# Optimization experiments

Measured on AMD Instinct MI355X. Metric: run time of the kernel, lower is better.

## Reference

```python
import jax, jax.numpy as jnp
import numpy as np

B, S, D, H, DH = 2, 2048, 2048, 16, 128
ROT_DIM = 128
ROT_BASE = 10000.0
ATTN_SCALE = float(np.sqrt(DH))


def _sin_cos_rotary(n_ctx, rotary_dim, base):
    pos = jnp.arange(n_ctx, dtype=jnp.float32)
    dim = jnp.arange(rotary_dim // 2, dtype=jnp.float32)
    freq = base ** (dim / (rotary_dim / 2))
    freq = jnp.concatenate([freq, freq])  # non-adjacent pairs: '(2 d)' layout
    angles = pos[:, None] / freq[None, :]  # [n_ctx, rotary_dim]
    return jnp.sin(angles), jnp.cos(angles)


def _rotate_every_two(x):
    # non-adjacent-pairs rotation: [-x2, x1] on halves of last dim
    d = x.shape[-1]
    return jnp.concatenate([-x[..., d // 2:], x[..., :d // 2]], axis=-1)


def _apply_rotary(x, sin, cos):
    # x: [batch, pos, head, d_head]
    n = x.shape[1]
    x_rot = x[..., :ROT_DIM]
    x_pass = x[..., ROT_DIM:]
    c = cos[:n][None, :, None, :]
    s = sin[:n][None, :, None, :]
    x_rotated = x_rot * c + _rotate_every_two(x_rot) * s
    return jnp.concatenate([x_rotated, x_pass], axis=-1)


def setup_inputs() -> dict:
    key = jax.random.key(0)
    ks = jax.random.split(key, 8)
    init = 0.02
    return {
        'query_input': jax.random.normal(ks[0], (B, S, D), jnp.float32),
        'key_input': jax.random.normal(ks[1], (B, S, D), jnp.float32),
        'value_input': jax.random.normal(ks[2], (B, S, D), jnp.float32),
        'W_Q': jax.random.normal(ks[3], (H, D, DH), jnp.float32) * init,
        'W_K': jax.random.normal(ks[4], (H, D, DH), jnp.float32) * init,
        'W_V': jax.random.normal(ks[5], (H, D, DH), jnp.float32) * init,
        'W_O': jax.random.normal(ks[6], (H, DH, D), jnp.float32) * init,
        'b_Q': jnp.zeros((H, DH), jnp.float32),
        'b_K': jnp.zeros((H, DH), jnp.float32),
        'b_V': jnp.zeros((H, DH), jnp.float32),
        'b_O': jnp.zeros((D,), jnp.float32),
    }


def reference(query_input, key_input, value_input, W_Q, W_K, W_V, W_O, b_Q, b_K, b_V, b_O):
    # QKV projections: [b, pos, d_model] x [h, d_model, d_head] -> [b, pos, h, d_head]
    q = jnp.einsum('bpd,hde->bphe', query_input, W_Q) + b_Q
    k = jnp.einsum('bpd,hde->bphe', key_input, W_K) + b_K
    v = jnp.einsum('bpd,hde->bphe', value_input, W_V) + b_V

    sin, cos = _sin_cos_rotary(S, ROT_DIM, ROT_BASE)
    q = _apply_rotary(q, sin, cos)
    k = _apply_rotary(k, sin, cos)

    # attention scores [b, h, q_pos, k_pos]
    scores = jnp.einsum('bqhe,bkhe->bhqk', q, k) / ATTN_SCALE
    causal = jnp.tril(jnp.ones((S, S), bool))
    scores = jnp.where(causal[None, None], scores, -jnp.inf)
    pattern = jax.nn.softmax(scores, axis=-1)
    pattern = jnp.where(jnp.isnan(pattern), jnp.zeros_like(pattern), pattern)

    z = jnp.einsum('bhqk,bkhe->bqhe', pattern, v)
    out = jnp.einsum('bqhe,hed->bqd', z, W_O) + b_O
    return out
```

## Files before the change

kernel.cpp:

```cpp
#include <hip/hip_runtime.h>
#include <hip/hip_bf16.h>
#include <cmath>

typedef __bf16 bf16;
typedef __bf16 bf16x8 __attribute__((ext_vector_type(8)));
typedef __bf16 bf16x4 __attribute__((ext_vector_type(4)));
typedef float  f32x4  __attribute__((ext_vector_type(4)));


__global__ void prep_kernel(const float* __restrict__ qin, const float* __restrict__ kin,
                            const float* __restrict__ vin,
                            const float* __restrict__ WQ, const float* __restrict__ WK,
                            const float* __restrict__ WV, const float* __restrict__ WO,
                            bf16* __restrict__ XQ, bf16* __restrict__ XK, bf16* __restrict__ XV,
                            bf16* __restrict__ WQT, bf16* __restrict__ WKT,
                            bf16* __restrict__ WVT, bf16* __restrict__ WOT) {
    int y = blockIdx.y;
    int o = blockIdx.x * 256 + threadIdx.x;
    if (y == 0) {
        int i = o * 2;
        float2 a = *(const float2*)(qin + i);
        float2 b = *(const float2*)(kin + i);
        float2 c = *(const float2*)(vin + i);
        bf16 ra[2] = { (bf16)a.x, (bf16)a.y };
        bf16 rb[2] = { (bf16)b.x, (bf16)b.y };
        bf16 rc[2] = { (bf16)c.x, (bf16)c.y };
        *(short*)&XQ[i] = *(short*)&ra[0]; *(short*)&XQ[i+1] = *(short*)&ra[1];
        *(short*)&XK[i] = *(short*)&rb[0]; *(short*)&XK[i+1] = *(short*)&rb[1];
        *(short*)&XV[i] = *(short*)&rc[0]; *(short*)&XV[i+1] = *(short*)&rc[1];
    } else if (y < 4) {
        const float* W = (y == 1) ? WQ : (y == 2) ? WK : WV;
        bf16* Wt       = (y == 1) ? WQT : (y == 2) ? WKT : WVT;
        int d = o & 2047;
        int he = o >> 11;
        int e = he & 127, h = he >> 7;
        Wt[o] = (bf16)W[(h << 18) + (d << 7) + e];
    } else {
        int he = o & 2047;
        int d = o >> 11;
        WOT[o] = (bf16)WO[(he << 11) + d];
    }
}

__launch_bounds__(256)
__global__ void qkv_gemm_kernel(const bf16* __restrict__ XQ, const bf16* __restrict__ XK,
                                const bf16* __restrict__ XV,
                                const bf16* __restrict__ WQT, const bf16* __restrict__ WKT,
                                const bf16* __restrict__ WVT,
                                const float* __restrict__ bQ, const float* __restrict__ bK,
                                const float* __restrict__ bV,
                                bf16* __restrict__ QB, bf16* __restrict__ KB,
                                bf16* __restrict__ VT) {
    __shared__ __align__(16) bf16 As[128 * 32];
    __shared__ __align__(16) bf16 Bs[128 * 32];
    __shared__ __align__(16) bf16 Cs[64 * 136];
    const int z = blockIdx.z;
    const bf16* A  = (z == 0) ? XQ  : (z == 1) ? XK  : XV;
    const bf16* Bm = (z == 0) ? WQT : (z == 1) ? WKT : WVT;
    const float* bias = (z == 0) ? bQ : (z == 1) ? bK : bV;

    const int tid = threadIdx.x;
    const int w = tid >> 6, lane = tid & 63;
    const int quad = lane >> 4, l16 = lane & 15;
    const int wm = w & 1, wn = w >> 1;
    const int m_base = blockIdx.x << 7, n_base = blockIdx.y << 7;

    const int srow = lane >> 2;
    const int scol = (lane & 3) << 3;
    const int ab0 = w * 2, ab1 = w * 2 + 1;
    const bf16* gA0 = A  + (long)(m_base + ab0 * 16 + srow) * 2048 + scol;
    const bf16* gA1 = A  + (long)(m_base + ab1 * 16 + srow) * 2048 + scol;
    const bf16* gB0 = Bm + (long)(n_base + ab0 * 16 + srow) * 2048 + scol;
    const bf16* gB1 = Bm + (long)(n_base + ab1 * 16 + srow) * 2048 + scol;
    bf16* lA0 = &As[ab0 * 512];
    bf16* lA1 = &As[ab1 * 512];
    bf16* lB0 = &Bs[ab0 * 512];
    bf16* lB1 = &Bs[ab1 * 512];

    f32x4 acc[4][4] = {};

    for (int k0 = 0; k0 < 2048; k0 += 32) {
        __builtin_amdgcn_global_load_lds((const __attribute__((address_space(1))) void*)(gA0 + k0),
                                         (__attribute__((address_space(3))) void*)lA0, 16, 0, 0);
        __builtin_amdgcn_global_load_lds((const __attribute__((address_space(1))) void*)(gA1 + k0),
                                         (__attribute__((address_space(3))) void*)lA1, 16, 0, 0);
        __builtin_amdgcn_global_load_lds((const __attribute__((address_space(1))) void*)(gB0 + k0),
                                         (__attribute__((address_space(3))) void*)lB0, 16, 0, 0);
        __builtin_amdgcn_global_load_lds((const __attribute__((address_space(1))) void*)(gB1 + k0),
                                         (__attribute__((address_space(3))) void*)lB1, 16, 0, 0);
        __syncthreads();

        bf16x8 af[4], bfr[4];
#pragma unroll
        for (int mt = 0; mt < 4; mt++)
            af[mt] = *(const bf16x8*)&As[((wm * 64 + mt * 16 + l16) << 5) + (quad << 3)];
#pragma unroll
        for (int nt = 0; nt < 4; nt++) {
            int nrow = wn * 32 + (nt & 1) * 16 + (nt >> 1) * 64 + l16;
            bfr[nt] = *(const bf16x8*)&Bs[(nrow << 5) + (quad << 3)];
        }
#pragma unroll
        for (int mt = 0; mt < 4; mt++)
#pragma unroll
            for (int nt = 0; nt < 4; nt++)
                acc[mt][nt] = __builtin_amdgcn_mfma_f32_16x16x32_bf16(af[mt], bfr[nt], acc[mt][nt], 0, 0, 0);
        __syncthreads();
    }

    const int bq = m_base >> 11;
    const int h  = n_base >> 7;
    const long obase = ((long)(bq * 16 + h)) << 18;

    if (z <= 1) {
        bf16* O = (z == 0) ? QB : KB;
        const float scl = (z == 0) ? 0.08838834764831845f : 1.0f;
#pragma unroll
        for (int nt = 0; nt < 2; nt++) {
            const int e_lo = wn * 32 + nt * 16 + l16;
            const float bv_lo = bias[n_base + e_lo];
            const float bv_hi = bias[n_base + e_lo + 64];
            const float inv_freq = exp2f((float)e_lo * -0.20762050593046f);
#pragma unroll
            for (int mt = 0; mt < 4; mt++) {
#pragma unroll
                for (int r = 0; r < 4; r++) {
                    int s = (m_base & 2047) + wm * 64 + mt * 16 + quad * 4 + r;
                    float sn, cs;
                    __sincosf((float)s * inv_freq, &sn, &cs);
                    float x0 = acc[mt][nt][r]     + bv_lo;
                    float x1 = acc[mt][nt + 2][r] + bv_hi;
                    O[obase + ((long)s << 7) + e_lo]      = (bf16)((x0 * cs - x1 * sn) * scl);
                    O[obase + ((long)s << 7) + e_lo + 64] = (bf16)((x1 * cs + x0 * sn) * scl);
                }
            }
        }
    } else {
#pragma unroll
        for (int eh = 0; eh < 2; eh++) {
#pragma unroll
            for (int nt2 = 0; nt2 < 2; nt2++) {
                const int nt = eh * 2 + nt2;
                const int e_l = wn * 32 + nt2 * 16 + l16;
                const float bv = bias[n_base + eh * 64 + e_l];
#pragma unroll
                for (int mt = 0; mt < 4; mt++) {
                    int s0 = wm * 64 + mt * 16 + quad * 4;
                    bf16x4 pk = { (bf16)(acc[mt][nt][0] + bv), (bf16)(acc[mt][nt][1] + bv),
                                  (bf16)(acc[mt][nt][2] + bv), (bf16)(acc[mt][nt][3] + bv) };
                    *(bf16x4*)&Cs[e_l * 136 + s0] = pk;
                }
            }
            __syncthreads();
            {
                const int e_l = tid >> 2;
                const int sq  = (tid & 3) << 5;
                const int e   = eh * 64 + e_l;
                const long vb = obase + ((long)e << 11) + (m_base & 2047) + sq;
#pragma unroll
                for (int j = 0; j < 4; j++)
                    *(bf16x8*)&VT[vb + j * 8] = *(const bf16x8*)&Cs[e_l * 136 + sq + j * 8];
            }
            __syncthreads();
        }
    }
}

__launch_bounds__(256, 3)
__global__ void flash_kernel(const bf16* __restrict__ Q, const bf16* __restrict__ K,
                             const bf16* __restrict__ Vt, bf16* __restrict__ Z) {
    __shared__ __align__(16) bf16 Ks[64 * 136];
    __shared__ __align__(16) bf16 Vs[128 * 72];
    __shared__ __align__(16) bf16 Ps[64 * 72];
    const int tid = threadIdx.x, w = tid >> 6, lane = tid & 63;
    const int quad = lane >> 4, l16 = lane & 15;
    const int n = blockIdx.x;
    const int bh = (n & 7) | (((n >> 3) & 3) << 3);
    const int qt = 31 - (n >> 5);
    const int b = bh >> 4, h = bh & 15;
    const long qk_base = (long)bh << 18;
    const int qbase = qt << 6;
    const float FM = 12.0f;

    const int kr_row = tid >> 4;
    const int kr_col = (tid & 15) << 3;
    const int vr_row = tid >> 3;
    const int vr_col = (tid & 7) << 3;
    const bf16* Kg = K  + qk_base + (long)kr_row * 128 + kr_col;
    const bf16* Vg = Vt + qk_base + (long)vr_row * 2048 + vr_col;

    bf16x8 qf[4];
#pragma unroll
    for (int ks = 0; ks < 4; ks++)
        qf[ks] = *(const bf16x8*)(Q + qk_base + ((long)(qbase + w * 16 + l16) << 7) + ks * 32 + (quad << 3));

    bf16x8 va[4], ka[4], vb2[4], kb[4];
#pragma unroll
    for (int p = 0; p < 4; p++) va[p] = *(const bf16x8*)(Vg + (long)p * 65536);
#pragma unroll
    for (int p = 0; p < 4; p++) ka[p] = *(const bf16x8*)(Kg + (long)(p * 16) * 128);

    f32x4 o[8] = {};
    float lsum[4] = {0.f, 0.f, 0.f, 0.f};

    for (int kt = 0; kt <= qt; kt++) {
#pragma unroll
        for (int p = 0; p < 4; p++)
            *(bf16x8*)&Vs[(p * 32 + vr_row) * 72 + vr_col] = va[p];
#pragma unroll
        for (int p = 0; p < 4; p++)
            *(bf16x8*)&Ks[(p * 16 + kr_row) * 136 + kr_col] = ka[p];
        if (kt < qt) {
            const long koff = (long)(kt + 1) * 64;
#pragma unroll
            for (int p = 0; p < 4; p++) vb2[p] = *(const bf16x8*)(Vg + (long)p * 65536 + koff);
#pragma unroll
            for (int p = 0; p < 4; p++) kb[p] = *(const bf16x8*)(Kg + (koff + p * 16) * 128);
        }
        __syncthreads();

        f32x4 sc[4] = {};
#pragma unroll
        for (int nt = 0; nt < 4; nt++)
#pragma unroll
            for (int ks = 0; ks < 4; ks++) {
                bf16x8 kf = *(const bf16x8*)&Ks[(nt * 16 + l16) * 136 + ks * 32 + (quad << 3)];
                sc[nt] = __builtin_amdgcn_mfma_f32_16x16x32_bf16(qf[ks], kf, sc[nt], 0, 0, 0);
            }

        if (kt == qt) {
#pragma unroll
            for (int nt = 0; nt < 4; nt++)
#pragma unroll
                for (int r = 0; r < 4; r++) {
                    int qrow = qbase + w * 16 + quad * 4 + r;
                    int kv = (qt << 6) + nt * 16 + l16;
                    if (kv > qrow) sc[nt][r] = -3.0e38f;
                }
        }

#pragma unroll
        for (int nt = 0; nt < 4; nt++)
#pragma unroll
            for (int r = 0; r < 4; r++) {
                float p = __expf(sc[nt][r] - FM);
                lsum[r] += p;
                Ps[(w * 16 + quad * 4 + r) * 72 + nt * 16 + l16] = (bf16)p;
            }

#pragma unroll
        for (int kk = 0; kk < 2; kk++) {
            bf16x8 pf = *(const bf16x8*)&Ps[(w * 16 + l16) * 72 + kk * 32 + (quad << 3)];
#pragma unroll
            for (int dt = 0; dt < 8; dt++) {
                bf16x8 vf = *(const bf16x8*)&Vs[(dt * 16 + l16) * 72 + kk * 32 + (quad << 3)];
                o[dt] = __builtin_amdgcn_mfma_f32_16x16x32_bf16(pf, vf, o[dt], 0, 0, 0);
            }
        }
        __syncthreads();

#pragma unroll
        for (int p = 0; p < 4; p++) va[p] = vb2[p];
#pragma unroll
        for (int p = 0; p < 4; p++) ka[p] = kb[p];
    }

#pragma unroll
    for (int r = 0; r < 4; r++) {
        float l = lsum[r];
        l += __shfl_xor(l, 1);
        l += __shfl_xor(l, 2);
        l += __shfl_xor(l, 4);
        l += __shfl_xor(l, 8);
        float inv = 1.f / l;
        int qrow = qbase + w * 16 + quad * 4 + r;
        long zr = ((long)(b * 2048 + qrow) << 11) + h * 128;
#pragma unroll
        for (int dt = 0; dt < 8; dt++)
            Z[zr + dt * 16 + l16] = (bf16)(o[dt][r] * inv);
    }
}

__launch_bounds__(256)
__global__ void gemm_o_kernel(const bf16* __restrict__ A, const bf16* __restrict__ Bm,
                              const float* __restrict__ bias, float* __restrict__ Of) {
    __shared__ __align__(16) bf16 As[128 * 32];
    __shared__ __align__(16) bf16 Bs[128 * 32];
    const int tid = threadIdx.x;
    const int w = tid >> 6, lane = tid & 63;
    const int quad = lane >> 4, l16 = lane & 15;
    const int wm = w & 1, wn = w >> 1;
    const int m_base = blockIdx.x << 7, n_base = blockIdx.y << 7;

    const int srow = lane >> 2;
    const int scol = (lane & 3) << 3;
    const int ab0 = w * 2, ab1 = w * 2 + 1;
    const bf16* gA0 = A  + (long)(m_base + ab0 * 16 + srow) * 2048 + scol;
    const bf16* gA1 = A  + (long)(m_base + ab1 * 16 + srow) * 2048 + scol;
    const bf16* gB0 = Bm + (long)(n_base + ab0 * 16 + srow) * 2048 + scol;
    const bf16* gB1 = Bm + (long)(n_base + ab1 * 16 + srow) * 2048 + scol;
    bf16* lA0 = &As[ab0 * 512];
    bf16* lA1 = &As[ab1 * 512];
    bf16* lB0 = &Bs[ab0 * 512];
    bf16* lB1 = &Bs[ab1 * 512];

    f32x4 acc[4][4] = {};

    for (int k0 = 0; k0 < 2048; k0 += 32) {
        __builtin_amdgcn_global_load_lds((const __attribute__((address_space(1))) void*)(gA0 + k0),
                                         (__attribute__((address_space(3))) void*)lA0, 16, 0, 0);
        __builtin_amdgcn_global_load_lds((const __attribute__((address_space(1))) void*)(gA1 + k0),
                                         (__attribute__((address_space(3))) void*)lA1, 16, 0, 0);
        __builtin_amdgcn_global_load_lds((const __attribute__((address_space(1))) void*)(gB0 + k0),
                                         (__attribute__((address_space(3))) void*)lB0, 16, 0, 0);
        __builtin_amdgcn_global_load_lds((const __attribute__((address_space(1))) void*)(gB1 + k0),
                                         (__attribute__((address_space(3))) void*)lB1, 16, 0, 0);
        __syncthreads();

        bf16x8 af[4], bfr[4];
#pragma unroll
        for (int mt = 0; mt < 4; mt++)
            af[mt] = *(const bf16x8*)&As[((wm * 64 + mt * 16 + l16) << 5) + (quad << 3)];
#pragma unroll
        for (int nt = 0; nt < 4; nt++)
            bfr[nt] = *(const bf16x8*)&Bs[((wn * 64 + nt * 16 + l16) << 5) + (quad << 3)];
#pragma unroll
        for (int mt = 0; mt < 4; mt++)
#pragma unroll
            for (int nt = 0; nt < 4; nt++)
                acc[mt][nt] = __builtin_amdgcn_mfma_f32_16x16x32_bf16(af[mt], bfr[nt], acc[mt][nt], 0, 0, 0);
        __syncthreads();
    }

#pragma unroll
    for (int nt = 0; nt < 4; nt++) {
        int col = n_base + wn * 64 + nt * 16 + l16;
        float bv = bias[col];
#pragma unroll
        for (int mt = 0; mt < 4; mt++) {
#pragma unroll
            for (int r = 0; r < 4; r++) {
                int row = m_base + wm * 64 + mt * 16 + quad * 4 + r;
                Of[((long)row << 11) + col] = acc[mt][nt][r] + bv;
            }
        }
    }
}

extern "C" void kernel_launch(void* const* d_in, const int* in_sizes, int n_in,
                              void* d_out, int out_size, void* d_ws, size_t ws_size,
                              hipStream_t stream) {
    (void)in_sizes; (void)n_in; (void)out_size; (void)ws_size;
    const float* qin = (const float*)d_in[0];
    const float* kin = (const float*)d_in[1];
    const float* vin = (const float*)d_in[2];
    const float* WQ  = (const float*)d_in[3];
    const float* WK  = (const float*)d_in[4];
    const float* WV  = (const float*)d_in[5];
    const float* WO  = (const float*)d_in[6];
    const float* bQ  = (const float*)d_in[7];
    const float* bK  = (const float*)d_in[8];
    const float* bV  = (const float*)d_in[9];
    const float* bO  = (const float*)d_in[10];
    float* out = (float*)d_out;

    bf16* ws = (bf16*)d_ws;
    bf16* XQ  = ws + 0L;
    bf16* XK  = ws + 8388608L;
    bf16* XV  = ws + 16777216L;
    bf16* WQT = ws + 25165824L;
    bf16* WKT = ws + 29360128L;
    bf16* WVT = ws + 33554432L;
    bf16* WOT = ws + 37748736L;
    bf16* QB  = ws + 41943040L;
    bf16* KB  = ws + 50331648L;
    bf16* VT  = ws + 58720256L;
    bf16* Z   = XQ;

    prep_kernel<<<dim3(16384, 5), 256, 0, stream>>>(qin, kin, vin, WQ, WK, WV, WO,
                                                    XQ, XK, XV, WQT, WKT, WVT, WOT);
    qkv_gemm_kernel<<<dim3(32, 16, 3), 256, 0, stream>>>(XQ, XK, XV, WQT, WKT, WVT,
                                                         bQ, bK, bV, QB, KB, VT);
    flash_kernel<<<1024, 256, 0, stream>>>(QB, KB, VT, Z);
    gemm_o_kernel<<<dim3(32, 16), 256, 0, stream>>>(Z, WOT, bO, out);
}
```

Before: 476.2 us.

## Split prep into vectorized convert and tiled transpose; register-prefetch padded GEMM tiles

The single prep kernel is replaced by two kernels. One converts the activations to bf16 with float4 loads. The other transposes the weights through a padded shared-memory tile so that both reads and writes are coalesced, replacing the strided per-element gathers. The QKV and output GEMMs drop the direct global-to-LDS loads and instead prefetch the next K-slice into registers while computing the current one. They store into LDS rows padded to 40 elements to avoid bank conflicts and declare launch bounds asking for 3 blocks per CU. This costs more registers and an extra store into LDS.

```diff
diff --git a/kernel.cpp b/kernel.cpp
--- a/kernel.cpp
+++ b/kernel.cpp
@@ -8,41 +8,70 @@
 typedef float  f32x4  __attribute__((ext_vector_type(4)));
 
 
-__global__ void prep_kernel(const float* __restrict__ qin, const float* __restrict__ kin,
-                            const float* __restrict__ vin,
-                            const float* __restrict__ WQ, const float* __restrict__ WK,
-                            const float* __restrict__ WV, const float* __restrict__ WO,
-                            bf16* __restrict__ XQ, bf16* __restrict__ XK, bf16* __restrict__ XV,
-                            bf16* __restrict__ WQT, bf16* __restrict__ WKT,
-                            bf16* __restrict__ WVT, bf16* __restrict__ WOT) {
-    int y = blockIdx.y;
-    int o = blockIdx.x * 256 + threadIdx.x;
-    if (y == 0) {
-        int i = o * 2;
-        float2 a = *(const float2*)(qin + i);
-        float2 b = *(const float2*)(kin + i);
-        float2 c = *(const float2*)(vin + i);
-        bf16 ra[2] = { (bf16)a.x, (bf16)a.y };
-        bf16 rb[2] = { (bf16)b.x, (bf16)b.y };
-        bf16 rc[2] = { (bf16)c.x, (bf16)c.y };
-        *(short*)&XQ[i] = *(short*)&ra[0]; *(short*)&XQ[i+1] = *(short*)&ra[1];
-        *(short*)&XK[i] = *(short*)&rb[0]; *(short*)&XK[i+1] = *(short*)&rb[1];
-        *(short*)&XV[i] = *(short*)&rc[0]; *(short*)&XV[i+1] = *(short*)&rc[1];
-    } else if (y < 4) {
-        const float* W = (y == 1) ? WQ : (y == 2) ? WK : WV;
-        bf16* Wt       = (y == 1) ? WQT : (y == 2) ? WKT : WVT;
-        int d = o & 2047;
-        int he = o >> 11;
-        int e = he & 127, h = he >> 7;
-        Wt[o] = (bf16)W[(h << 18) + (d << 7) + e];
+__global__ void xcvt_kernel(const float* __restrict__ a, const float* __restrict__ b,
+                            const float* __restrict__ c,
+                            bf16* __restrict__ oa, bf16* __restrict__ ob, bf16* __restrict__ oc) {
+    int i = (blockIdx.x * 256 + threadIdx.x) * 4;
+    float4 va = *(const float4*)(a + i);
+    float4 vb = *(const float4*)(b + i);
+    float4 vc = *(const float4*)(c + i);
+    bf16x4 ra = { (bf16)va.x, (bf16)va.y, (bf16)va.z, (bf16)va.w };
+    bf16x4 rb = { (bf16)vb.x, (bf16)vb.y, (bf16)vb.z, (bf16)vb.w };
+    bf16x4 rc = { (bf16)vc.x, (bf16)vc.y, (bf16)vc.z, (bf16)vc.w };
+    *(bf16x4*)(oa + i) = ra;
+    *(bf16x4*)(ob + i) = rb;
+    *(bf16x4*)(oc + i) = rc;
+}
+
+__global__ void wtr_kernel(const float* __restrict__ WQ, const float* __restrict__ WK,
+                           const float* __restrict__ WV, const float* __restrict__ WO,
+                           bf16* __restrict__ WQT, bf16* __restrict__ WKT,
+                           bf16* __restrict__ WVT, bf16* __restrict__ WOT) {
+    __shared__ float T[64 * 65];
+    const int z = blockIdx.y;
+    const int bx = blockIdx.x;
+    const int tid = threadIdx.x;
+    const int tr = tid >> 4;
+    const int tc = (tid & 15) * 4;
+
+    const float* src; bf16* dst;
+    long sbase, dbase; int sRS;
+    if (z < 3) {
+        src = (z == 0) ? WQ : (z == 1) ? WK : WV;
+        dst = (z == 0) ? WQT : (z == 1) ? WKT : WVT;
+        int h = bx >> 6, rem = bx & 63;
+        int d0 = (rem >> 1) << 6, e0 = (rem & 1) << 6;
+        sbase = (long)h * 262144 + (long)d0 * 128 + e0;
+        sRS = 128;
+        dbase = (long)(h * 128 + e0) * 2048 + d0;
     } else {
-        int he = o & 2047;
-        int d = o >> 11;
-        WOT[o] = (bf16)WO[(he << 11) + d];
-    }
-}
-
-__launch_bounds__(256)
+        src = WO; dst = WOT;
+        int a0 = (bx >> 5) << 6, b0 = (bx & 31) << 6;
+        sbase = (long)a0 * 2048 + b0;
+        sRS = 2048;
+        dbase = (long)b0 * 2048 + a0;
+    }
+
+#pragma unroll
+    for (int p = 0; p < 4; p++) {
+        int r = p * 16 + tr;
+        float4 v = *(const float4*)(src + sbase + (long)r * sRS + tc);
+        T[r * 65 + tc]     = v.x;
+        T[r * 65 + tc + 1] = v.y;
+        T[r * 65 + tc + 2] = v.z;
+        T[r * 65 + tc + 3] = v.w;
+    }
+    __syncthreads();
+#pragma unroll
+    for (int p = 0; p < 4; p++) {
+        int rr = p * 16 + tr;
+        bf16x4 o = { (bf16)T[tc * 65 + rr],       (bf16)T[(tc + 1) * 65 + rr],
+                     (bf16)T[(tc + 2) * 65 + rr], (bf16)T[(tc + 3) * 65 + rr] };
+        *(bf16x4*)(dst + dbase + (long)rr * 2048 + tc) = o;
+    }
+}
+
+__launch_bounds__(256, 3)
 __global__ void qkv_gemm_kernel(const bf16* __restrict__ XQ, const bf16* __restrict__ XK,
                                 const bf16* __restrict__ XV,
                                 const bf16* __restrict__ WQT, const bf16* __restrict__ WKT,
@@ -51,8 +80,8 @@
                                 const float* __restrict__ bV,
                                 bf16* __restrict__ QB, bf16* __restrict__ KB,
                                 bf16* __restrict__ VT) {
-    __shared__ __align__(16) bf16 As[128 * 32];
-    __shared__ __align__(16) bf16 Bs[128 * 32];
+    __shared__ __align__(16) bf16 As[128 * 40];
+    __shared__ __align__(16) bf16 Bs[128 * 40];
     __shared__ __align__(16) bf16 Cs[64 * 136];
     const int z = blockIdx.z;
     const bf16* A  = (z == 0) ? XQ  : (z == 1) ? XK  : XV;
@@ -65,39 +94,42 @@
     const int wm = w & 1, wn = w >> 1;
     const int m_base = blockIdx.x << 7, n_base = blockIdx.y << 7;
 
-    const int srow = lane >> 2;
-    const int scol = (lane & 3) << 3;
-    const int ab0 = w * 2, ab1 = w * 2 + 1;
-    const bf16* gA0 = A  + (long)(m_base + ab0 * 16 + srow) * 2048 + scol;
-    const bf16* gA1 = A  + (long)(m_base + ab1 * 16 + srow) * 2048 + scol;
-    const bf16* gB0 = Bm + (long)(n_base + ab0 * 16 + srow) * 2048 + scol;
-    const bf16* gB1 = Bm + (long)(n_base + ab1 * 16 + srow) * 2048 + scol;
-    bf16* lA0 = &As[ab0 * 512];
-    bf16* lA1 = &As[ab1 * 512];
-    bf16* lB0 = &Bs[ab0 * 512];
-    bf16* lB1 = &Bs[ab1 * 512];
+    const int srow = tid >> 2;
+    const int scol = (tid & 3) << 3;
+    const bf16* gA = A  + (long)(m_base + srow) * 2048 + scol;
+    const bf16* gB = Bm + (long)(n_base + srow) * 2048 + scol;
 
     f32x4 acc[4][4] = {};
+    bf16x8 ar[2], br[2], arn[2], brn[2];
+#pragma unroll
+    for (int p = 0; p < 2; p++) {
+        ar[p] = *(const bf16x8*)(gA + (long)p * 64 * 2048);
+        br[p] = *(const bf16x8*)(gB + (long)p * 64 * 2048);
+    }
 
     for (int k0 = 0; k0 < 2048; k0 += 32) {
-        __builtin_amdgcn_global_load_lds((const __attribute__((address_space(1))) void*)(gA0 + k0),
-                                         (__attribute__((address_space(3))) void*)lA0, 16, 0, 0);
-        __builtin_amdgcn_global_load_lds((const __attribute__((address_space(1))) void*)(gA1 + k0),
-                                         (__attribute__((address_space(3))) void*)lA1, 16, 0, 0);
-        __builtin_amdgcn_global_load_lds((const __attribute__((address_space(1))) void*)(gB0 + k0),
-                                         (__attribute__((address_space(3))) void*)lB0, 16, 0, 0);
-        __builtin_amdgcn_global_load_lds((const __attribute__((address_space(1))) void*)(gB1 + k0),
-                                         (__attribute__((address_space(3))) void*)lB1, 16, 0, 0);
+#pragma unroll
+        for (int p = 0; p < 2; p++) {
+            *(bf16x8*)&As[(p * 64 + srow) * 40 + scol] = ar[p];
+            *(bf16x8*)&Bs[(p * 64 + srow) * 40 + scol] = br[p];
+        }
+        if (k0 + 32 < 2048) {
+#pragma unroll
+            for (int p = 0; p < 2; p++) {
+                arn[p] = *(const bf16x8*)(gA + (long)p * 64 * 2048 + k0 + 32);
+                brn[p] = *(const bf16x8*)(gB + (long)p * 64 * 2048 + k0 + 32);
+            }
+        }
         __syncthreads();
 
         bf16x8 af[4], bfr[4];
 #pragma unroll
         for (int mt = 0; mt < 4; mt++)
-            af[mt] = *(const bf16x8*)&As[((wm * 64 + mt * 16 + l16) << 5) + (quad << 3)];
+            af[mt] = *(const bf16x8*)&As[(wm * 64 + mt * 16 + l16) * 40 + (quad << 3)];
 #pragma unroll
         for (int nt = 0; nt < 4; nt++) {
             int nrow = wn * 32 + (nt & 1) * 16 + (nt >> 1) * 64 + l16;
-            bfr[nt] = *(const bf16x8*)&Bs[(nrow << 5) + (quad << 3)];
+            bfr[nt] = *(const bf16x8*)&Bs[nrow * 40 + (quad << 3)];
         }
 #pragma unroll
         for (int mt = 0; mt < 4; mt++)
@@ -105,6 +137,9 @@
             for (int nt = 0; nt < 4; nt++)
                 acc[mt][nt] = __builtin_amdgcn_mfma_f32_16x16x32_bf16(af[mt], bfr[nt], acc[mt][nt], 0, 0, 0);
         __syncthreads();
+
+#pragma unroll
+        for (int p = 0; p < 2; p++) { ar[p] = arn[p]; br[p] = brn[p]; }
     }
 
     const int bq = m_base >> 11;
@@ -280,55 +315,61 @@
     }
 }
 
-__launch_bounds__(256)
+__launch_bounds__(256, 3)
 __global__ void gemm_o_kernel(const bf16* __restrict__ A, const bf16* __restrict__ Bm,
                               const float* __restrict__ bias, float* __restrict__ Of) {
-    __shared__ __align__(16) bf16 As[128 * 32];
-    __shared__ __align__(16) bf16 Bs[128 * 32];
+    __shared__ __align__(16) bf16 As[128 * 40];
+    __shared__ __align__(16) bf16 Bs[128 * 40];
     const int tid = threadIdx.x;
     const int w = tid >> 6, lane = tid & 63;
     const int quad = lane >> 4, l16 = lane & 15;
     const int wm = w & 1, wn = w >> 1;
     const int m_base = blockIdx.x << 7, n_base = blockIdx.y << 7;
 
-    const int srow = lane >> 2;
-    const int scol = (lane & 3) << 3;
-    const int ab0 = w * 2, ab1 = w * 2 + 1;
-    const bf16* gA0 = A  + (long)(m_base + ab0 * 16 + srow) * 2048 + scol;
-    const bf16* gA1 = A  + (long)(m_base + ab1 * 16 + srow) * 2048 + scol;
-    const bf16* gB0 = Bm + (long)(n_base + ab0 * 16 + srow) * 2048 + scol;
-    const bf16* gB1 = Bm + (long)(n_base + ab1 * 16 + srow) * 2048 + scol;
-    bf16* lA0 = &As[ab0 * 512];
-    bf16* lA1 = &As[ab1 * 512];
-    bf16* lB0 = &Bs[ab0 * 512];
-    bf16* lB1 = &Bs[ab1 * 512];
+    const int srow = tid >> 2;
+    const int scol = (tid & 3) << 3;
+    const bf16* gA = A  + (long)(m_base + srow) * 2048 + scol;
+    const bf16* gB = Bm + (long)(n_base + srow) * 2048 + scol;
 
     f32x4 acc[4][4] = {};
+    bf16x8 ar[2], br[2], arn[2], brn[2];
+#pragma unroll
+    for (int p = 0; p < 2; p++) {
+        ar[p] = *(const bf16x8*)(gA + (long)p * 64 * 2048);
+        br[p] = *(const bf16x8*)(gB + (long)p * 64 * 2048);
+    }
 
     for (int k0 = 0; k0 < 2048; k0 += 32) {
-        __builtin_amdgcn_global_load_lds((const __attribute__((address_space(1))) void*)(gA0 + k0),
-                                         (__attribute__((address_space(3))) void*)lA0, 16, 0, 0);
-        __builtin_amdgcn_global_load_lds((const __attribute__((address_space(1))) void*)(gA1 + k0),
-                                         (__attribute__((address_space(3))) void*)lA1, 16, 0, 0);
-        __builtin_amdgcn_global_load_lds((const __attribute__((address_space(1))) void*)(gB0 + k0),
-                                         (__attribute__((address_space(3))) void*)lB0, 16, 0, 0);
-        __builtin_amdgcn_global_load_lds((const __attribute__((address_space(1))) void*)(gB1 + k0),
-                                         (__attribute__((address_space(3))) void*)lB1, 16, 0, 0);
+#pragma unroll
+        for (int p = 0; p < 2; p++) {
+            *(bf16x8*)&As[(p * 64 + srow) * 40 + scol] = ar[p];
+            *(bf16x8*)&Bs[(p * 64 + srow) * 40 + scol] = br[p];
+        }
+        if (k0 + 32 < 2048) {
+#pragma unroll
+            for (int p = 0; p < 2; p++) {
+                arn[p] = *(const bf16x8*)(gA + (long)p * 64 * 2048 + k0 + 32);
+                brn[p] = *(const bf16x8*)(gB + (long)p * 64 * 2048 + k0 + 32);
+            }
+        }
         __syncthreads();
 
         bf16x8 af[4], bfr[4];
 #pragma unroll
         for (int mt = 0; mt < 4; mt++)
-            af[mt] = *(const bf16x8*)&As[((wm * 64 + mt * 16 + l16) << 5) + (quad << 3)];
+            af[mt] = *(const bf16x8*)&As[(wm * 64 + mt * 16 + l16) * 40 + (quad << 3)];
 #pragma unroll
         for (int nt = 0; nt < 4; nt++)
-            bfr[nt] = *(const bf16x8*)&Bs[((wn * 64 + nt * 16 + l16) << 5) + (quad << 3)];
+            bfr[nt] = *(const bf16x8*)&Bs[(wn * 64 + nt * 16 + l16) * 40 + (quad << 3)];
 #pragma unroll
         for (int mt = 0; mt < 4; mt++)
 #pragma unroll
             for (int nt = 0; nt < 4; nt++)
                 acc[mt][nt] = __builtin_amdgcn_mfma_f32_16x16x32_bf16(af[mt], bfr[nt], acc[mt][nt], 0, 0, 0);
         __syncthreads();
+
+#pragma unroll
+        for (int p = 0; p < 2; p++) { ar[p] = arn[p]; br[p] = brn[p]; }
     }
 
 #pragma unroll
@@ -376,8 +417,8 @@
     bf16* VT  = ws + 58720256L;
     bf16* Z   = XQ;
 
-    prep_kernel<<<dim3(16384, 5), 256, 0, stream>>>(qin, kin, vin, WQ, WK, WV, WO,
-                                                    XQ, XK, XV, WQT, WKT, WVT, WOT);
+    xcvt_kernel<<<8192, 256, 0, stream>>>(qin, kin, vin, XQ, XK, XV);
+    wtr_kernel<<<dim3(1024, 4), 256, 0, stream>>>(WQ, WK, WV, WO, WQT, WKT, WVT, WOT);
     qkv_gemm_kernel<<<dim3(32, 16, 3), 256, 0, stream>>>(XQ, XK, XV, WQT, WKT, WVT,
                                                          bQ, bK, bV, QB, KB, VT);
     flash_kernel<<<1024, 256, 0, stream>>>(QB, KB, VT, Z);
```

Measured after the change: 427.3 us. 1.11x faster.
